# Kernel tuning notes

Measured on AMD Instinct MI355X. Metric: run time of the kernel, lower is better.

The kernel has to match this reference:

```python
import jax, jax.numpy as jnp
import numpy as np

DIM = 1024
HEADS = 16
HEAD_DIM = DIM // HEADS
SCALE = HEAD_DIM ** -0.5


def setup_inputs() -> dict:
    key = jax.random.key(0)
    ks = jax.random.split(key, 6)
    B, N = 2, 2048
    s = DIM ** -0.5
    return {
        "x": jax.random.normal(ks[0], (B, N, DIM), dtype=jnp.float32),
        "Wq": jax.random.normal(ks[1], (DIM, DIM), dtype=jnp.float32) * s,
        "Wk": jax.random.normal(ks[2], (DIM, DIM), dtype=jnp.float32) * s,
        "Wv": jax.random.normal(ks[3], (DIM, DIM), dtype=jnp.float32) * s,
        "Wo": jax.random.normal(ks[4], (DIM, DIM), dtype=jnp.float32) * s,
        "bo": jnp.zeros((DIM,), dtype=jnp.float32),
    }


def reference(x, Wq, Wk, Wv, Wo, bo):
    B, N, D = x.shape
    # Linear projections (torch Linear: y = x @ W.T)
    q = x @ Wq.T
    k = x @ Wk.T
    v = x @ Wv.T
    # [B, H, N, hd]
    q = q.reshape(B, N, HEADS, HEAD_DIM).transpose(0, 2, 1, 3)
    k = k.reshape(B, N, HEADS, HEAD_DIM).transpose(0, 2, 1, 3)
    v = v.reshape(B, N, HEADS, HEAD_DIM).transpose(0, 2, 1, 3)
    scores = jnp.einsum('bhid,bhjd->bhij', q, k) * SCALE
    probs = jax.nn.softmax(scores, axis=-1)
    out = jnp.einsum('bhij,bhjd->bhid', probs, v)
    out = out.transpose(0, 2, 1, 3).reshape(B, N, D)
    return out @ Wo.T + bo
```

## Files before the change

kernel.cpp:

```cpp
#include <hip/hip_runtime.h>

#define DIM    1024
#define HEADS  16
#define HD     64
#define BATCH  2
#define SEQ    2048
#define C2     0.18033688011112042f

typedef __attribute__((ext_vector_type(8))) short           short8;
typedef __attribute__((ext_vector_type(4))) float           f4;
typedef __attribute__((ext_vector_type(4))) unsigned short  u16x4;
typedef __attribute__((ext_vector_type(4))) unsigned int    u32x4;
typedef __attribute__((ext_vector_type(2))) unsigned int    u32x2;

typedef __attribute__((address_space(3))) unsigned int       as3_u32;
typedef const __attribute__((address_space(1))) unsigned int as1_u32;

__device__ __forceinline__ unsigned short f2bf(float f) {
    unsigned int u = __builtin_bit_cast(unsigned int, f);
    u = (u + 0x7fffu + ((u >> 16) & 1u)) >> 16;
    return (unsigned short)u;
}
__device__ __forceinline__ unsigned int pk_bf16(float a, float b) {
    return (unsigned int)f2bf(a) | ((unsigned int)f2bf(b) << 16);
}

#if __has_builtin(__builtin_amdgcn_exp2f)
#define EXP2(x) __builtin_amdgcn_exp2f(x)
#else
#define EXP2(x) exp2f(x)
#endif

__device__ __forceinline__ void gl2lds16(const unsigned short* g, unsigned short* l) {
    __builtin_amdgcn_global_load_lds((as1_u32*)g, (as3_u32*)l, 16, 0, 0);
}

__global__ __launch_bounds__(256) void k_cast_all(
    const float* __restrict__ x,  const float* __restrict__ wq,
    const float* __restrict__ wk, const float* __restrict__ wv,
    const float* __restrict__ wo, unsigned short* __restrict__ dst)
{
    const int i = blockIdx.x * 256 + threadIdx.x;
    const float* src;
    int off;
    if (i < (1 << 20))            { src = x;  off = 0; }
    else if (i < (5 << 18))       { src = wq; off = 1 << 20; }
    else if (i < (6 << 18))       { src = wk; off = 5 << 18; }
    else if (i < (7 << 18))       { src = wv; off = 6 << 18; }
    else                          { src = wo; off = 7 << 18; }
    f4 v = ((const f4*)src)[i - off];
    u16x4 o;
    o[0] = f2bf(v[0]); o[1] = f2bf(v[1]); o[2] = f2bf(v[2]); o[3] = f2bf(v[3]);
    ((u16x4*)dst)[i] = o;
}

__global__ __launch_bounds__(256) void gemm_qkv(
    const unsigned short* __restrict__ A,
    const unsigned short* __restrict__ Wq,
    const unsigned short* __restrict__ Wk,
    const unsigned short* __restrict__ Wv,
    unsigned short* __restrict__ Qo,
    unsigned short* __restrict__ Ko,
    unsigned short* __restrict__ Vo)
{
    __shared__ __align__(16) unsigned short As[128 * 32];
    __shared__ __align__(16) unsigned short Bs[128 * 32];
    const int wsel = blockIdx.x >> 3;
    const unsigned short* W = (wsel == 0) ? Wq : ((wsel == 1) ? Wk : Wv);
    const int m0 = blockIdx.y * 128, n0 = (blockIdx.x & 7) * 128;
    const int tid  = threadIdx.x;
    const int wave = tid >> 6, lane = tid & 63;
    const int quad = lane >> 4, l16 = lane & 15;
    const int wm = (wave & 1) << 6, wn = (wave >> 1) << 6;

    f4 acc[4][4] = {};

    for (int k0 = 0; k0 < DIM; k0 += 32) {
        __syncthreads();
        #pragma unroll
        for (int i = 0; i < 2; i++) {
            const int c = tid + (i << 8);
            const int row = c >> 2, koff = (c & 3) << 3;
            gl2lds16(&A[(size_t)(m0 + row) * DIM + k0 + koff], &As[(size_t)((i << 8) + (wave << 6)) * 8]);
            gl2lds16(&W[(size_t)(n0 + row) * DIM + k0 + koff], &Bs[(size_t)((i << 8) + (wave << 6)) * 8]);
        }
        __syncthreads();
        short8 afr[4], bfr[4];
        #pragma unroll
        for (int i = 0; i < 4; i++)
            afr[i] = *(const short8*)(&As[(wm + i * 16 + l16) * 32 + quad * 8]);
        #pragma unroll
        for (int j = 0; j < 4; j++)
            bfr[j] = *(const short8*)(&Bs[(wn + j * 16 + l16) * 32 + quad * 8]);
        #pragma unroll
        for (int i = 0; i < 4; i++)
            #pragma unroll
            for (int j = 0; j < 4; j++)
                acc[i][j] = __builtin_amdgcn_mfma_f32_16x16x32_bf16(afr[i], bfr[j], acc[i][j], 0, 0, 0);
    }

    unsigned short* out = (wsel == 0) ? Qo : ((wsel == 1) ? Ko : Vo);
    #pragma unroll
    for (int j = 0; j < 4; j++) {
        const int n = n0 + wn + j * 16 + l16;
        const int h = n >> 6, d = n & (HD - 1);
        #pragma unroll
        for (int i = 0; i < 4; i++) {
            const int mb = m0 + wm + i * 16 + quad * 4;
            const int b = mb >> 11, ns = mb & (SEQ - 1);
            if (wsel == 2) {
                u32x2 pw;
                pw[0] = pk_bf16(acc[i][j][0], acc[i][j][1]);
                pw[1] = pk_bf16(acc[i][j][2], acc[i][j][3]);
                *(u32x2*)(&out[((size_t)(b * HEADS + h) * HD + d) * SEQ + ns]) = pw;
            } else {
                const float sc = (wsel == 0) ? C2 : 1.0f;
                #pragma unroll
                for (int r = 0; r < 4; r++)
                    out[((size_t)(b * HEADS + h) * SEQ + ns + r) * HD + d] = f2bf(acc[i][j][r] * sc);
            }
        }
    }
}

__global__ __launch_bounds__(256) void attn_fwd(
    const unsigned short* __restrict__ Qg,
    const unsigned short* __restrict__ Kg,
    const unsigned short* __restrict__ VTg,
    unsigned short* __restrict__ AOb)
{
    __shared__ __align__(16) unsigned short QsP[64 * 72];
    __shared__ __align__(16) unsigned short Ks [64 * 72];
    __shared__ __align__(16) unsigned short VsT[64 * 72];

    const int bh = blockIdx.y;
    const int q0 = blockIdx.x << 6;
    const unsigned short* Qb  = Qg  + (size_t)bh * SEQ * HD;
    const unsigned short* Kb  = Kg  + (size_t)bh * SEQ * HD;
    const unsigned short* VTb = VTg + (size_t)bh * HD * SEQ;

    const int tid  = threadIdx.x;
    const int wave = tid >> 6, lane = tid & 63;
    const int quad = lane >> 4, l16 = lane & 15;
    const int qw   = wave << 4;
    const int r8   = tid >> 3;
    const int g8   = (tid & 7) * 8;

    #pragma unroll
    for (int p = 0; p < 2; p++) {
        const int row = r8 + p * 32;
        *(u32x4*)(&QsP[row * 72 + g8]) = *(const u32x4*)(&Qb[(size_t)(q0 + row) * HD + g8]);
        *(u32x4*)(&Ks [row * 72 + g8]) = *(const u32x4*)(&Kb [(size_t)row * HD + g8]);
        *(u32x4*)(&VsT[row * 72 + g8]) = *(const u32x4*)(&VTb[(size_t)row * SEQ + g8]);
    }
    __syncthreads();

    short8 qf[2];
    #pragma unroll
    for (int ks = 0; ks < 2; ks++)
        qf[ks] = *(const short8*)(&QsP[(qw + l16) * 72 + ks * 32 + quad * 8]);

    f4 lsum = {};
    f4 Oacc[4] = {};

    for (int kt = 0; kt < SEQ / 64; kt++) {
        u32x4 kpre[2], vpre[2];
        if (kt < SEQ / 64 - 1) {
            #pragma unroll
            for (int p = 0; p < 2; p++) {
                const int row = r8 + p * 32;
                kpre[p] = *(const u32x4*)(&Kb [(size_t)((kt + 1) * 64 + row) * HD + g8]);
                vpre[p] = *(const u32x4*)(&VTb[(size_t)row * SEQ + (kt + 1) * 64 + g8]);
            }
        }

        f4 sacc[4] = {};
        #pragma unroll
        for (int ks = 0; ks < 2; ks++) {
            short8 kfr[4];
            #pragma unroll
            for (int mf = 0; mf < 4; mf++)
                kfr[mf] = *(const short8*)(&Ks[(mf * 16 + l16) * 72 + ks * 32 + quad * 8]);
            #pragma unroll
            for (int mf = 0; mf < 4; mf++)
                sacc[mf] = __builtin_amdgcn_mfma_f32_16x16x32_bf16(kfr[mf], qf[ks], sacc[mf], 0, 0, 0);
        }

        #pragma unroll
        for (int mf = 0; mf < 4; mf++) {
            f4 pv;
            #pragma unroll
            for (int r = 0; r < 4; r++)
                pv[r] = EXP2(sacc[mf][r]);
            lsum += pv;
            u32x2 pw;
            pw[0] = pk_bf16(pv[0], pv[1]);
            pw[1] = pk_bf16(pv[2], pv[3]);
            *(u32x2*)(&QsP[(qw + l16) * 72 + mf * 16 + quad * 4]) = pw;
        }

        #pragma unroll
        for (int ks = 0; ks < 2; ks++) {
            short8 vfr[4];
            #pragma unroll
            for (int mf = 0; mf < 4; mf++)
                vfr[mf] = *(const short8*)(&VsT[(mf * 16 + l16) * 72 + ks * 32 + quad * 8]);
            const short8 pf = *(const short8*)(&QsP[(qw + l16) * 72 + ks * 32 + quad * 8]);
            #pragma unroll
            for (int mf = 0; mf < 4; mf++)
                Oacc[mf] = __builtin_amdgcn_mfma_f32_16x16x32_bf16(vfr[mf], pf, Oacc[mf], 0, 0, 0);
        }

        __syncthreads();
        if (kt < SEQ / 64 - 1) {
            #pragma unroll
            for (int p = 0; p < 2; p++) {
                const int row = r8 + p * 32;
                *(u32x4*)(&Ks [row * 72 + g8]) = kpre[p];
                *(u32x4*)(&VsT[row * 72 + g8]) = vpre[p];
            }
        }
        __syncthreads();
    }

    float l = lsum[0] + lsum[1] + lsum[2] + lsum[3];
    l += __shfl_xor(l, 16);
    l += __shfl_xor(l, 32);
    const float inv = 1.0f / l;

    const int b = bh >> 4, h = bh & (HEADS - 1);
    const int qg = q0 + qw + l16;
    #pragma unroll
    for (int mf = 0; mf < 4; mf++) {
        u32x2 o;
        o[0] = pk_bf16(Oacc[mf][0] * inv, Oacc[mf][1] * inv);
        o[1] = pk_bf16(Oacc[mf][2] * inv, Oacc[mf][3] * inv);
        *(u32x2*)(&AOb[(size_t)(b * SEQ + qg) * DIM + h * HD + mf * 16 + quad * 4]) = o;
    }
}

__global__ __launch_bounds__(256) void gemm_out(
    const unsigned short* __restrict__ A,
    const unsigned short* __restrict__ W,
    float* __restrict__ out,
    const float* __restrict__ bias)
{
    __shared__ __align__(16) unsigned short As[64 * 32];
    __shared__ __align__(16) unsigned short Bs[128 * 32];
    const int m0 = blockIdx.y * 64, n0 = blockIdx.x * 128;
    const int tid  = threadIdx.x;
    const int wave = tid >> 6, lane = tid & 63;
    const int quad = lane >> 4, l16 = lane & 15;
    const int wm = (wave & 1) << 5, wn = (wave >> 1) << 6;

    f4 acc[2][4] = {};

    for (int k0 = 0; k0 < DIM; k0 += 32) {
        __syncthreads();
        gl2lds16(&A[(size_t)(m0 + (tid >> 2)) * DIM + k0 + ((tid & 3) << 3)],
                 &As[(size_t)(wave << 6) * 8]);
        #pragma unroll
        for (int i = 0; i < 2; i++) {
            const int c = tid + (i << 8);
            gl2lds16(&W[(size_t)(n0 + (c >> 2)) * DIM + k0 + ((c & 3) << 3)],
                     &Bs[(size_t)((i << 8) + (wave << 6)) * 8]);
        }
        __syncthreads();
        short8 afr[2], bfr[4];
        #pragma unroll
        for (int i = 0; i < 2; i++)
            afr[i] = *(const short8*)(&As[(wm + i * 16 + l16) * 32 + quad * 8]);
        #pragma unroll
        for (int j = 0; j < 4; j++)
            bfr[j] = *(const short8*)(&Bs[(wn + j * 16 + l16) * 32 + quad * 8]);
        #pragma unroll
        for (int i = 0; i < 2; i++)
            #pragma unroll
            for (int j = 0; j < 4; j++)
                acc[i][j] = __builtin_amdgcn_mfma_f32_16x16x32_bf16(afr[i], bfr[j], acc[i][j], 0, 0, 0);
    }

    #pragma unroll
    for (int j = 0; j < 4; j++) {
        const int n = n0 + wn + j * 16 + l16;
        const float bv = bias[n];
        #pragma unroll
        for (int i = 0; i < 2; i++) {
            #pragma unroll
            for (int r = 0; r < 4; r++) {
                const int m = m0 + wm + i * 16 + quad * 4 + r;
                out[(size_t)m * DIM + n] = acc[i][j][r] + bv;
            }
        }
    }
}

extern "C" void kernel_launch(void* const* d_in, const int* in_sizes, int n_in,
                              void* d_out, int out_size, void* d_ws, size_t ws_size,
                              hipStream_t stream) {
    (void)in_sizes; (void)n_in; (void)out_size; (void)ws_size;
    const float* x  = (const float*)d_in[0];
    const float* Wq = (const float*)d_in[1];
    const float* Wk = (const float*)d_in[2];
    const float* Wv = (const float*)d_in[3];
    const float* Wo = (const float*)d_in[4];
    const float* bo = (const float*)d_in[5];

    unsigned short* wsu = (unsigned short*)d_ws;
    unsigned short* xb  = wsu;
    unsigned short* Wqb = wsu + (4u  << 20);
    unsigned short* Wkb = wsu + (5u  << 20);
    unsigned short* Wvb = wsu + (6u  << 20);
    unsigned short* Wob = wsu + (7u  << 20);
    unsigned short* Qb  = wsu + (8u  << 20);
    unsigned short* Kb  = wsu + (12u << 20);
    unsigned short* VTb = wsu + (16u << 20);
    unsigned short* AOb = wsu + (20u << 20);

    k_cast_all<<<8192, 256, 0, stream>>>(x, Wq, Wk, Wv, Wo, wsu);

    gemm_qkv<<<dim3(24, 32), 256, 0, stream>>>(xb, Wqb, Wkb, Wvb, Qb, Kb, VTb);

    attn_fwd<<<dim3(SEQ / 64, BATCH * HEADS), 256, 0, stream>>>(Qb, Kb, VTb, AOb);

    gemm_out<<<dim3(8, 64), 256, 0, stream>>>(AOb, Wob, (float*)d_out, bo);
}
```

Before: 214.7 us.

## Widen attention Q tile, keep P in registers, swap GEMM operands for vector stores

The attention kernel now handles 128 queries per block, with each wave covering two 16-query fragments, so every K/V tile loaded into LDS is reused twice as much. When the 16x16x16 bf16 MFMA builtin exists, the probabilities stay in registers as its operands instead of taking an LDS write/read round trip. The QKV and output GEMMs swap their A/B operands for Q/K and the output projection, so each lane writes contiguous 4-element vectors (packed bf16 or float4 with a vector bias load) instead of scalar strided stores. In exchange the attention grid halves to 512 blocks and per-thread register use roughly doubles, which may lower occupancy.

```diff
diff --git a/kernel.cpp b/kernel.cpp
--- a/kernel.cpp
+++ b/kernel.cpp
@@ -8,6 +8,7 @@
 #define C2     0.18033688011112042f
 
 typedef __attribute__((ext_vector_type(8))) short           short8;
+typedef __attribute__((ext_vector_type(4))) short           short4v;
 typedef __attribute__((ext_vector_type(4))) float           f4;
 typedef __attribute__((ext_vector_type(4))) unsigned short  u16x4;
 typedef __attribute__((ext_vector_type(4))) unsigned int    u32x4;
@@ -63,16 +64,20 @@
     unsigned short* __restrict__ Ko,
     unsigned short* __restrict__ Vo)
 {
-    __shared__ __align__(16) unsigned short As[128 * 32];
-    __shared__ __align__(16) unsigned short Bs[128 * 32];
+    __shared__ __align__(16) unsigned short Xs[128 * 32];
+    __shared__ __align__(16) unsigned short Ws[128 * 32];
     const int wsel = blockIdx.x >> 3;
     const unsigned short* W = (wsel == 0) ? Wq : ((wsel == 1) ? Wk : Wv);
-    const int m0 = blockIdx.y * 128, n0 = (blockIdx.x & 7) * 128;
+    const int fb = (blockIdx.x & 7) * 128;
+    const int sb = blockIdx.y * 128;
     const int tid  = threadIdx.x;
     const int wave = tid >> 6, lane = tid & 63;
     const int quad = lane >> 4, l16 = lane & 15;
     const int wm = (wave & 1) << 6, wn = (wave >> 1) << 6;
 
+    const unsigned short* aLDS = (wsel < 2) ? Ws : Xs;
+    const unsigned short* bLDS = (wsel < 2) ? Xs : Ws;
+
     f4 acc[4][4] = {};
 
     for (int k0 = 0; k0 < DIM; k0 += 32) {
@@ -81,17 +86,17 @@
         for (int i = 0; i < 2; i++) {
             const int c = tid + (i << 8);
             const int row = c >> 2, koff = (c & 3) << 3;
-            gl2lds16(&A[(size_t)(m0 + row) * DIM + k0 + koff], &As[(size_t)((i << 8) + (wave << 6)) * 8]);
-            gl2lds16(&W[(size_t)(n0 + row) * DIM + k0 + koff], &Bs[(size_t)((i << 8) + (wave << 6)) * 8]);
+            gl2lds16(&A[(size_t)(sb + row) * DIM + k0 + koff], &Xs[(size_t)((i << 8) + (wave << 6)) * 8]);
+            gl2lds16(&W[(size_t)(fb + row) * DIM + k0 + koff], &Ws[(size_t)((i << 8) + (wave << 6)) * 8]);
         }
         __syncthreads();
         short8 afr[4], bfr[4];
         #pragma unroll
         for (int i = 0; i < 4; i++)
-            afr[i] = *(const short8*)(&As[(wm + i * 16 + l16) * 32 + quad * 8]);
+            afr[i] = *(const short8*)(&aLDS[(wm + i * 16 + l16) * 32 + quad * 8]);
         #pragma unroll
         for (int j = 0; j < 4; j++)
-            bfr[j] = *(const short8*)(&Bs[(wn + j * 16 + l16) * 32 + quad * 8]);
+            bfr[j] = *(const short8*)(&bLDS[(wn + j * 16 + l16) * 32 + quad * 8]);
         #pragma unroll
         for (int i = 0; i < 4; i++)
             #pragma unroll
@@ -99,25 +104,36 @@
                 acc[i][j] = __builtin_amdgcn_mfma_f32_16x16x32_bf16(afr[i], bfr[j], acc[i][j], 0, 0, 0);
     }
 
-    unsigned short* out = (wsel == 0) ? Qo : ((wsel == 1) ? Ko : Vo);
-    #pragma unroll
-    for (int j = 0; j < 4; j++) {
-        const int n = n0 + wn + j * 16 + l16;
-        const int h = n >> 6, d = n & (HD - 1);
-        #pragma unroll
-        for (int i = 0; i < 4; i++) {
-            const int mb = m0 + wm + i * 16 + quad * 4;
-            const int b = mb >> 11, ns = mb & (SEQ - 1);
-            if (wsel == 2) {
+    if (wsel < 2) {
+        unsigned short* out = (wsel == 0) ? Qo : Ko;
+        const float sc = (wsel == 0) ? C2 : 1.0f;
+        #pragma unroll
+        for (int j = 0; j < 4; j++) {
+            const int ms = sb + wn + j * 16 + l16;
+            const int b = ms >> 11, ns = ms & (SEQ - 1);
+            #pragma unroll
+            for (int i = 0; i < 4; i++) {
+                const int feat = fb + wm + i * 16 + quad * 4;
+                const int h = feat >> 6, d = feat & (HD - 1);
+                u32x2 pw;
+                pw[0] = pk_bf16(acc[i][j][0] * sc, acc[i][j][1] * sc);
+                pw[1] = pk_bf16(acc[i][j][2] * sc, acc[i][j][3] * sc);
+                *(u32x2*)(&out[((size_t)(b * HEADS + h) * SEQ + ns) * HD + d]) = pw;
+            }
+        }
+    } else {
+        #pragma unroll
+        for (int j = 0; j < 4; j++) {
+            const int feat = fb + wn + j * 16 + l16;
+            const int h = feat >> 6, d = feat & (HD - 1);
+            #pragma unroll
+            for (int i = 0; i < 4; i++) {
+                const int ms = sb + wm + i * 16 + quad * 4;
+                const int b = ms >> 11, ns = ms & (SEQ - 1);
                 u32x2 pw;
                 pw[0] = pk_bf16(acc[i][j][0], acc[i][j][1]);
                 pw[1] = pk_bf16(acc[i][j][2], acc[i][j][3]);
-                *(u32x2*)(&out[((size_t)(b * HEADS + h) * HD + d) * SEQ + ns]) = pw;
-            } else {
-                const float sc = (wsel == 0) ? C2 : 1.0f;
-                #pragma unroll
-                for (int r = 0; r < 4; r++)
-                    out[((size_t)(b * HEADS + h) * SEQ + ns + r) * HD + d] = f2bf(acc[i][j][r] * sc);
+                *(u32x2*)(&Vo[((size_t)(b * HEADS + h) * HD + d) * SEQ + ns]) = pw;
             }
         }
     }
@@ -129,12 +145,12 @@
     const unsigned short* __restrict__ VTg,
     unsigned short* __restrict__ AOb)
 {
-    __shared__ __align__(16) unsigned short QsP[64 * 72];
+    __shared__ __align__(16) unsigned short QsP[128 * 72];
     __shared__ __align__(16) unsigned short Ks [64 * 72];
     __shared__ __align__(16) unsigned short VsT[64 * 72];
 
     const int bh = blockIdx.y;
-    const int q0 = blockIdx.x << 6;
+    const int q0 = blockIdx.x << 7;
     const unsigned short* Qb  = Qg  + (size_t)bh * SEQ * HD;
     const unsigned short* Kb  = Kg  + (size_t)bh * SEQ * HD;
     const unsigned short* VTb = VTg + (size_t)bh * HD * SEQ;
@@ -142,26 +158,32 @@
     const int tid  = threadIdx.x;
     const int wave = tid >> 6, lane = tid & 63;
     const int quad = lane >> 4, l16 = lane & 15;
-    const int qw   = wave << 4;
+    const int qw   = wave << 5;
     const int r8   = tid >> 3;
     const int g8   = (tid & 7) * 8;
 
     #pragma unroll
+    for (int p = 0; p < 4; p++) {
+        const int row = r8 + p * 32;
+        *(u32x4*)(&QsP[row * 72 + g8]) = *(const u32x4*)(&Qb[(size_t)(q0 + row) * HD + g8]);
+    }
+    #pragma unroll
     for (int p = 0; p < 2; p++) {
         const int row = r8 + p * 32;
-        *(u32x4*)(&QsP[row * 72 + g8]) = *(const u32x4*)(&Qb[(size_t)(q0 + row) * HD + g8]);
         *(u32x4*)(&Ks [row * 72 + g8]) = *(const u32x4*)(&Kb [(size_t)row * HD + g8]);
         *(u32x4*)(&VsT[row * 72 + g8]) = *(const u32x4*)(&VTb[(size_t)row * SEQ + g8]);
     }
     __syncthreads();
 
-    short8 qf[2];
-    #pragma unroll
-    for (int ks = 0; ks < 2; ks++)
-        qf[ks] = *(const short8*)(&QsP[(qw + l16) * 72 + ks * 32 + quad * 8]);
-
-    f4 lsum = {};
-    f4 Oacc[4] = {};
+    short8 qf[2][2];
+    #pragma unroll
+    for (int nf = 0; nf < 2; nf++)
+        #pragma unroll
+        for (int ks = 0; ks < 2; ks++)
+            qf[nf][ks] = *(const short8*)(&QsP[(qw + nf * 16 + l16) * 72 + ks * 32 + quad * 8]);
+
+    f4 lsum[2] = {};
+    f4 Oacc[4][2] = {};
 
     for (int kt = 0; kt < SEQ / 64; kt++) {
         u32x4 kpre[2], vpre[2];
@@ -174,7 +196,7 @@
             }
         }
 
-        f4 sacc[4] = {};
+        f4 sacc[4][2] = {};
         #pragma unroll
         for (int ks = 0; ks < 2; ks++) {
             short8 kfr[4];
@@ -183,33 +205,73 @@
                 kfr[mf] = *(const short8*)(&Ks[(mf * 16 + l16) * 72 + ks * 32 + quad * 8]);
             #pragma unroll
             for (int mf = 0; mf < 4; mf++)
-                sacc[mf] = __builtin_amdgcn_mfma_f32_16x16x32_bf16(kfr[mf], qf[ks], sacc[mf], 0, 0, 0);
-        }
-
-        #pragma unroll
-        for (int mf = 0; mf < 4; mf++) {
-            f4 pv;
-            #pragma unroll
-            for (int r = 0; r < 4; r++)
-                pv[r] = EXP2(sacc[mf][r]);
-            lsum += pv;
-            u32x2 pw;
-            pw[0] = pk_bf16(pv[0], pv[1]);
-            pw[1] = pk_bf16(pv[2], pv[3]);
-            *(u32x2*)(&QsP[(qw + l16) * 72 + mf * 16 + quad * 4]) = pw;
-        }
-
+                #pragma unroll
+                for (int nf = 0; nf < 2; nf++)
+                    sacc[mf][nf] = __builtin_amdgcn_mfma_f32_16x16x32_bf16(kfr[mf], qf[nf][ks], sacc[mf][nf], 0, 0, 0);
+        }
+
+#if __has_builtin(__builtin_amdgcn_mfma_f32_16x16x16bf16_1k)
+        short4v pb[2][4];
+        #pragma unroll
+        for (int nf = 0; nf < 2; nf++) {
+            #pragma unroll
+            for (int mf = 0; mf < 4; mf++) {
+                f4 pv;
+                #pragma unroll
+                for (int r = 0; r < 4; r++)
+                    pv[r] = EXP2(sacc[mf][nf][r]);
+                lsum[nf] += pv;
+                short4v pk;
+                #pragma unroll
+                for (int r = 0; r < 4; r++)
+                    pk[r] = (short)f2bf(pv[r]);
+                pb[nf][mf] = pk;
+            }
+        }
+        #pragma unroll
+        for (int ks16 = 0; ks16 < 4; ks16++) {
+            short4v vfr[4];
+            #pragma unroll
+            for (int mf = 0; mf < 4; mf++)
+                vfr[mf] = *(const short4v*)(&VsT[(mf * 16 + l16) * 72 + ks16 * 16 + quad * 4]);
+            #pragma unroll
+            for (int mf = 0; mf < 4; mf++)
+                #pragma unroll
+                for (int nf = 0; nf < 2; nf++)
+                    Oacc[mf][nf] = __builtin_amdgcn_mfma_f32_16x16x16bf16_1k(vfr[mf], pb[nf][ks16], Oacc[mf][nf], 0, 0, 0);
+        }
+#else
+        #pragma unroll
+        for (int nf = 0; nf < 2; nf++) {
+            #pragma unroll
+            for (int mf = 0; mf < 4; mf++) {
+                f4 pv;
+                #pragma unroll
+                for (int r = 0; r < 4; r++)
+                    pv[r] = EXP2(sacc[mf][nf][r]);
+                lsum[nf] += pv;
+                u32x2 pw;
+                pw[0] = pk_bf16(pv[0], pv[1]);
+                pw[1] = pk_bf16(pv[2], pv[3]);
+                *(u32x2*)(&QsP[(qw + nf * 16 + l16) * 72 + mf * 16 + quad * 4]) = pw;
+            }
+        }
         #pragma unroll
         for (int ks = 0; ks < 2; ks++) {
-            short8 vfr[4];
+            short8 vfr[4], pf[2];
             #pragma unroll
             for (int mf = 0; mf < 4; mf++)
                 vfr[mf] = *(const short8*)(&VsT[(mf * 16 + l16) * 72 + ks * 32 + quad * 8]);
-            const short8 pf = *(const short8*)(&QsP[(qw + l16) * 72 + ks * 32 + quad * 8]);
-            #pragma unroll
-            for (int mf = 0; mf < 4; mf++)
-                Oacc[mf] = __builtin_amdgcn_mfma_f32_16x16x32_bf16(vfr[mf], pf, Oacc[mf], 0, 0, 0);
-        }
+            #pragma unroll
+            for (int nf = 0; nf < 2; nf++)
+                pf[nf] = *(const short8*)(&QsP[(qw + nf * 16 + l16) * 72 + ks * 32 + quad * 8]);
+            #pragma unroll
+            for (int mf = 0; mf < 4; mf++)
+                #pragma unroll
+                for (int nf = 0; nf < 2; nf++)
+                    Oacc[mf][nf] = __builtin_amdgcn_mfma_f32_16x16x32_bf16(vfr[mf], pf[nf], Oacc[mf][nf], 0, 0, 0);
+        }
+#endif
 
         __syncthreads();
         if (kt < SEQ / 64 - 1) {
@@ -223,31 +285,34 @@
         __syncthreads();
     }
 
-    float l = lsum[0] + lsum[1] + lsum[2] + lsum[3];
-    l += __shfl_xor(l, 16);
-    l += __shfl_xor(l, 32);
-    const float inv = 1.0f / l;
-
     const int b = bh >> 4, h = bh & (HEADS - 1);
-    const int qg = q0 + qw + l16;
-    #pragma unroll
-    for (int mf = 0; mf < 4; mf++) {
-        u32x2 o;
-        o[0] = pk_bf16(Oacc[mf][0] * inv, Oacc[mf][1] * inv);
-        o[1] = pk_bf16(Oacc[mf][2] * inv, Oacc[mf][3] * inv);
-        *(u32x2*)(&AOb[(size_t)(b * SEQ + qg) * DIM + h * HD + mf * 16 + quad * 4]) = o;
+    #pragma unroll
+    for (int nf = 0; nf < 2; nf++) {
+        float l = lsum[nf][0] + lsum[nf][1] + lsum[nf][2] + lsum[nf][3];
+        l += __shfl_xor(l, 16);
+        l += __shfl_xor(l, 32);
+        const float inv = 1.0f / l;
+        const int qg = q0 + qw + nf * 16 + l16;
+        #pragma unroll
+        for (int mf = 0; mf < 4; mf++) {
+            u32x2 o;
+            o[0] = pk_bf16(Oacc[mf][nf][0] * inv, Oacc[mf][nf][1] * inv);
+            o[1] = pk_bf16(Oacc[mf][nf][2] * inv, Oacc[mf][nf][3] * inv);
+            *(u32x2*)(&AOb[(size_t)(b * SEQ + qg) * DIM + h * HD + mf * 16 + quad * 4]) = o;
+        }
     }
 }
 
 __global__ __launch_bounds__(256) void gemm_out(
-    const unsigned short* __restrict__ A,
+    const unsigned short* __restrict__ AO,
     const unsigned short* __restrict__ W,
     float* __restrict__ out,
     const float* __restrict__ bias)
 {
     __shared__ __align__(16) unsigned short As[64 * 32];
     __shared__ __align__(16) unsigned short Bs[128 * 32];
-    const int m0 = blockIdx.y * 64, n0 = blockIdx.x * 128;
+    const int n0 = blockIdx.x * 128;
+    const int m0 = blockIdx.y * 64;
     const int tid  = threadIdx.x;
     const int wave = tid >> 6, lane = tid & 63;
     const int quad = lane >> 4, l16 = lane & 15;
@@ -257,12 +322,12 @@
 
     for (int k0 = 0; k0 < DIM; k0 += 32) {
         __syncthreads();
-        gl2lds16(&A[(size_t)(m0 + (tid >> 2)) * DIM + k0 + ((tid & 3) << 3)],
+        gl2lds16(&W[(size_t)(m0 + (tid >> 2)) * DIM + k0 + ((tid & 3) << 3)],
                  &As[(size_t)(wave << 6) * 8]);
         #pragma unroll
         for (int i = 0; i < 2; i++) {
             const int c = tid + (i << 8);
-            gl2lds16(&W[(size_t)(n0 + (c >> 2)) * DIM + k0 + ((c & 3) << 3)],
+            gl2lds16(&AO[(size_t)(n0 + (c >> 2)) * DIM + k0 + ((c & 3) << 3)],
                      &Bs[(size_t)((i << 8) + (wave << 6)) * 8]);
         }
         __syncthreads();
@@ -281,16 +346,13 @@
     }
 
     #pragma unroll
-    for (int j = 0; j < 4; j++) {
-        const int n = n0 + wn + j * 16 + l16;
-        const float bv = bias[n];
-        #pragma unroll
-        for (int i = 0; i < 2; i++) {
-            #pragma unroll
-            for (int r = 0; r < 4; r++) {
-                const int m = m0 + wm + i * 16 + quad * 4 + r;
-                out[(size_t)m * DIM + n] = acc[i][j][r] + bv;
-            }
+    for (int i = 0; i < 2; i++) {
+        const int feat = m0 + wm + i * 16 + quad * 4;
+        const f4 bv = *(const f4*)(&bias[feat]);
+        #pragma unroll
+        for (int j = 0; j < 4; j++) {
+            const int ns = n0 + wn + j * 16 + l16;
+            *(f4*)(&out[(size_t)ns * DIM + feat]) = acc[i][j] + bv;
         }
     }
 }
@@ -321,7 +383,7 @@
 
     gemm_qkv<<<dim3(24, 32), 256, 0, stream>>>(xb, Wqb, Wkb, Wvb, Qb, Kb, VTb);
 
-    attn_fwd<<<dim3(SEQ / 64, BATCH * HEADS), 256, 0, stream>>>(Qb, Kb, VTb, AOb);
-
-    gemm_out<<<dim3(8, 64), 256, 0, stream>>>(AOb, Wob, (float*)d_out, bo);
-}
+    attn_fwd<<<dim3(SEQ / 128, BATCH * HEADS), 256, 0, stream>>>(Qb, Kb, VTb, AOb);
+
+    gemm_out<<<dim3(32, 16), 256, 0, stream>>>(AOb, Wob, (float*)d_out, bo);
+}
```

Result: faster. 196.8 us (-8.4%).
